# Optimization experiments

Measured on AMD Instinct MI355X. Metric: run time of the kernel, lower is better.

The kernel has to match this reference:

```python
import jax, jax.numpy as jnp
import numpy as np

N_NODES = 100000
N_EDGES = 1000000
N_FEAT = 136
HIDDEN = 64
N_CLASSES = 2
NUM_GRAPHS = 512


def setup_inputs() -> dict:
    key = jax.random.key(0)
    ks = jax.random.split(key, 8)
    x = jax.random.normal(ks[0], (N_NODES, N_FEAT), dtype=jnp.float32)
    edge_index = jax.random.randint(ks[1], (2, N_EDGES), 0, N_NODES, dtype=jnp.int64)
    batch = jnp.sort(jax.random.randint(ks[2], (N_NODES,), 0, NUM_GRAPHS, dtype=jnp.int64))
    W1 = jax.random.normal(ks[3], (N_FEAT, HIDDEN), dtype=jnp.float32) * (1.0 / np.sqrt(N_FEAT))
    b1 = jnp.zeros((HIDDEN,), dtype=jnp.float32)
    W2 = jax.random.normal(ks[4], (HIDDEN, HIDDEN), dtype=jnp.float32) * (1.0 / np.sqrt(HIDDEN))
    b2 = jnp.zeros((HIDDEN,), dtype=jnp.float32)
    Wout = jax.random.normal(ks[5], (HIDDEN, N_CLASSES), dtype=jnp.float32) * (1.0 / np.sqrt(HIDDEN))
    bout = jnp.zeros((N_CLASSES,), dtype=jnp.float32)
    return {"x": x, "edge_index": edge_index, "batch": batch,
            "W1": W1, "b1": b1, "W2": W2, "b2": b2, "Wout": Wout, "bout": bout}


def _gcn_conv(x, src, dst, W, b, n_nodes):
    # GCNConv: D^{-1/2} (A+I) D^{-1/2} X W + b (self-loops already appended in src/dst)
    h = x @ W                                           # [N, out]
    ones = jnp.ones(src.shape, dtype=h.dtype)
    deg = jax.ops.segment_sum(ones, dst, num_segments=n_nodes)  # in-degree incl. self-loop
    dinv = jnp.where(deg > 0, jax.lax.rsqrt(deg), 0.0)
    norm = dinv[src] * dinv[dst]                        # [E]
    msg = h[src] * norm[:, None]                        # gather + normalize
    out = jax.ops.segment_sum(msg, dst, num_segments=n_nodes)   # scatter-add
    return out + b


def reference(x, edge_index, batch, W1, b1, W2, b2, Wout, bout):
    n = x.shape[0]
    loops = jnp.arange(n, dtype=edge_index.dtype)
    src = jnp.concatenate([edge_index[0], loops])
    dst = jnp.concatenate([edge_index[1], loops])

    h = jax.nn.relu(_gcn_conv(x, src, dst, W1, b1, n))
    # dropout p=0.5 is identity in eval mode
    h = jax.nn.relu(_gcn_conv(h, src, dst, W2, b2, n))

    # global_mean_pool over batch segments
    sums = jax.ops.segment_sum(h, batch, num_segments=NUM_GRAPHS)       # [G, H]
    counts = jax.ops.segment_sum(jnp.ones((n,), h.dtype), batch, num_segments=NUM_GRAPHS)
    pooled = sums / jnp.maximum(counts, 1.0)[:, None]

    return pooled @ Wout + bout                                         # [G, C]
```

## Files before the change

### kernel.cpp

```cpp
#include <hip/hip_runtime.h>
#include <hip/hip_bf16.h>

#define N_NODES   100000
#define N_EDGES   1000000
#define N_FEAT    136
#define HIDDEN    64
#define N_CLASSES 2
#define NUM_GRAPHS 512

#define NP_PAD    100352
#define SCAN_BLKS 98

#define EPW       128
#define NWAVE     7813
#define E_PAD     (NWAVE * EPW)
#define SEG_BLOCKS ((NWAVE + 3) / 4)

#define K1_4 (N_FEAT / 4)
#define K2_4 (HIDDEN / 4)

#define K1PAD 160
#define K2PAD 72

#define NB_E    ((N_EDGES + 255) / 256)
#define NB_SC   ((N_EDGES / 4 + 255) / 256)
#define NB_HIST (NB_E + 3)
#define NB_MM   ((N_NODES + 63) / 64)
#define FUSED_GRID 5474

typedef unsigned short ushort_t;
typedef __attribute__((ext_vector_type(8))) short bf16x8;
typedef __attribute__((ext_vector_type(4))) float f32x4;
typedef __attribute__((ext_vector_type(4))) int i32x4;
typedef __attribute__((ext_vector_type(4))) unsigned short u16x4;

__device__ __forceinline__ ushort_t f2b(float v) {
    unsigned b = __float_as_uint(v);
    return (ushort_t)((b + 0x7FFF + ((b >> 16) & 1)) >> 16);
}
__device__ __forceinline__ float b2f(ushort_t u) {
    return __uint_as_float(((unsigned)u) << 16);
}
__device__ __forceinline__ unsigned pack2(float a, float b) {
    return (unsigned)f2b(a) | ((unsigned)f2b(b) << 16);
}

__global__ __launch_bounds__(256) void fused_hist_mm1_kernel(
        const int* __restrict__ dst, int* __restrict__ cnt,
        ushort_t* __restrict__ rank,
        const int* __restrict__ batch, int* __restrict__ gstart,
        const float* __restrict__ x, const float* __restrict__ W1,
        ushort_t* __restrict__ tpb) {
    __shared__ ushort_t wtb[64 * K1PAD];
    int t = threadIdx.x;
    int gq = blockIdx.x / 7, gr = blockIdx.x % 7;

    if (gr >= 2) {
        int hb = gq * 5 + (gr - 2);
        if (hb >= NB_HIST) return;
        if (hb >= NB_E) {
            int g = (hb - NB_E) * 256 + t;
            if (g <= NUM_GRAPHS) {
                int lo = 0, hi = N_NODES;
                while (lo < hi) {
                    int mid = (lo + hi) >> 1;
                    if (batch[mid] < g) lo = mid + 1; else hi = mid;
                }
                gstart[g] = lo;
            }
            return;
        }
        int e = hb * 256 + t;
        if (e < N_EDGES) {
            int d = __builtin_nontemporal_load(&dst[e]);
            int r = atomicAdd(&cnt[d], 1);
            __builtin_nontemporal_store((ushort_t)r, &rank[e]);
        }
        return;
    }

    int mb = gq * 2 + gr;
    if (mb >= NB_MM) return;
    int n0 = mb * 64;
    {
        for (int i = t; i < N_FEAT * HIDDEN; i += 256) {
            int n = i & 63, k = i >> 6;
            wtb[n * K1PAD + k] = f2b(W1[i]);
        }
        for (int i = t; i < 64 * 12; i += 256) {
            int n = i / 12, c = i % 12;
            *(unsigned*)&wtb[n * K1PAD + N_FEAT + 2 * c] = 0;
        }
    }
    __syncthreads();
    int w = t >> 6, lane = t & 63;
    int quad = lane >> 4, l16 = lane & 15;
    int an = n0 + w * 16 + l16; if (an >= N_NODES) an = N_NODES - 1;
    const f32x4* xr = (const f32x4*)(x + (long long)an * N_FEAT);
    f32x4 acc[4] = {{0,0,0,0},{0,0,0,0},{0,0,0,0},{0,0,0,0}};
#pragma unroll
    for (int kc = 0; kc < K1PAD / 32; ++kc) {
        int k0 = kc * 32 + quad * 8;
        bf16x8 a = {0, 0, 0, 0, 0, 0, 0, 0};
        if (k0 < N_FEAT) {
            f32x4 u0 = __builtin_nontemporal_load(&xr[kc * 8 + quad * 2]);
            f32x4 u1 = __builtin_nontemporal_load(&xr[kc * 8 + quad * 2 + 1]);
            union { bf16x8 v; unsigned u[4]; } cv;
            cv.u[0] = pack2(u0.x, u0.y);
            cv.u[1] = pack2(u0.z, u0.w);
            cv.u[2] = pack2(u1.x, u1.y);
            cv.u[3] = pack2(u1.z, u1.w);
            a = cv.v;
        }
#pragma unroll
        for (int nt = 0; nt < 4; ++nt) {
            bf16x8 b = *(const bf16x8*)&wtb[(nt * 16 + l16) * K1PAD + kc * 32 + quad * 8];
            acc[nt] = __builtin_amdgcn_mfma_f32_16x16x32_bf16(a, b, acc[nt], 0, 0, 0);
        }
    }
#pragma unroll
    for (int r = 0; r < 4; ++r) {
        int nl = w * 16 + quad * 4 + r;
        int node = n0 + nl;
        if (node < N_NODES) {
#pragma unroll
            for (int nt = 0; nt < 4; ++nt)
                tpb[node * 64 + nt * 16 + l16] = f2b(acc[nt][r]);
        }
    }
}

__global__ __launch_bounds__(256) void scan1_kernel(const int* __restrict__ cnt,
                                                    int* __restrict__ row_ptr,
                                                    int* __restrict__ partials) {
    __shared__ int sd[256];
    int b = blockIdx.x, t = threadIdx.x;
    int i0 = b * 1024 + t * 4;
    int c0 = (i0 + 0 < N_NODES) ? cnt[i0 + 0] : 0;
    int c1 = (i0 + 1 < N_NODES) ? cnt[i0 + 1] : 0;
    int c2 = (i0 + 2 < N_NODES) ? cnt[i0 + 2] : 0;
    int c3 = (i0 + 3 < N_NODES) ? cnt[i0 + 3] : 0;
    int tsum = c0 + c1 + c2 + c3;
    sd[t] = tsum;
    __syncthreads();
    for (int off = 1; off < 256; off <<= 1) {
        int v = (t >= off) ? sd[t - off] : 0;
        __syncthreads();
        sd[t] += v;
        __syncthreads();
    }
    int excl = sd[t] - tsum;
    row_ptr[i0 + 0] = excl;
    row_ptr[i0 + 1] = excl + c0;
    row_ptr[i0 + 2] = excl + c0 + c1;
    row_ptr[i0 + 3] = excl + c0 + c1 + c2;
    if (t == 255) partials[b] = sd[255];
}

__global__ __launch_bounds__(128) void scan2_kernel(int* __restrict__ partials) {
    __shared__ int sd[128];
    int t = threadIdx.x;
    int v = (t < SCAN_BLKS) ? partials[t] : 0;
    sd[t] = v;
    __syncthreads();
    for (int off = 1; off < 128; off <<= 1) {
        int u = (t >= off) ? sd[t - off] : 0;
        __syncthreads();
        sd[t] += u;
        __syncthreads();
    }
    partials[t] = sd[t] - v;
}

__global__ __launch_bounds__(256) void scan3_kernel(int* __restrict__ row_ptr,
                                                    const int* __restrict__ cnt,
                                                    const int* __restrict__ partials,
                                                    int* __restrict__ dst_sorted,
                                                    int* __restrict__ csr_src,
                                                    float* __restrict__ dinv) {
    int i = blockIdx.x * 256 + threadIdx.x;
    if (i < N_NODES) {
        int v = row_ptr[i] + partials[i >> 10];
        int deg = cnt[i];
        row_ptr[i] = v;
        dinv[i] = rsqrtf((float)(deg + 1));
        for (int j = v; j < v + deg; ++j) dst_sorted[j] = i;
    }
    if (i == N_NODES) {
        row_ptr[N_NODES] = N_EDGES;
        for (int j = N_EDGES; j < E_PAD; ++j) {
            dst_sorted[j] = N_NODES;
            csr_src[j] = 0;
        }
    }
}

__global__ __launch_bounds__(256) void scatter_kernel(const int* __restrict__ src,
                                                      const int* __restrict__ dst,
                                                      const ushort_t* __restrict__ rank,
                                                      const int* __restrict__ row_ptr,
                                                      int* __restrict__ csr_src) {
    int e0 = (blockIdx.x * 256 + threadIdx.x) * 4;
    if (e0 >= N_EDGES) return;
    i32x4 s4 = __builtin_nontemporal_load((const i32x4*)&src[e0]);
    i32x4 d4 = __builtin_nontemporal_load((const i32x4*)&dst[e0]);
    u16x4 r4 = *(const u16x4*)&rank[e0];
    int p0 = row_ptr[d4.x] + (int)r4.x;
    int p1 = row_ptr[d4.y] + (int)r4.y;
    int p2 = row_ptr[d4.z] + (int)r4.z;
    int p3 = row_ptr[d4.w] + (int)r4.w;
    csr_src[p0] = s4.x;
    csr_src[p1] = s4.y;
    csr_src[p2] = s4.z;
    csr_src[p3] = s4.w;
}

__global__ __launch_bounds__(256) void mm2_kernel(float* __restrict__ agg,
                                                  ushort_t* __restrict__ tpb,
                                                  const float* __restrict__ W2,
                                                  const float* __restrict__ dinv,
                                                  const float* __restrict__ bias) {
    __shared__ ushort_t hsb[64 * K2PAD];
    __shared__ ushort_t wtb[64 * K2PAD];
    __shared__ float    dsv[64];
    __shared__ float    bsv[64];
    int t = threadIdx.x;
    int n0 = blockIdx.x * 64;
    if (t < 64) {
        int n = n0 + t; if (n >= N_NODES) n = N_NODES - 1;
        dsv[t] = dinv[n];
        bsv[t] = bias[t];
    }
    __syncthreads();
    {
        for (int i = t; i < HIDDEN * HIDDEN; i += 256) {
            int n = i & 63, k = i >> 6;
            wtb[n * K2PAD + k] = f2b(W2[i]);
        }
        for (int i = t; i < 64 * 4; i += 256) {
            int n = i / 4, c = i % 4;
            *(unsigned*)&wtb[n * K2PAD + HIDDEN + 2 * c] = 0;
        }
        for (int i = t; i < 64 * 16; i += 256) {
            int r = i >> 4, c = i & 15;
            int n_raw = n0 + r;
            int n = (n_raw < N_NODES) ? n_raw : N_NODES - 1;
            float4 va = ((const float4*)agg)[n * 16 + c];
            uint2 ut = *(const uint2*)&tpb[n * 64 + c * 4];
            float di = dsv[r];
            float s0 = b2f((ushort_t)(ut.x & 0xffff)) * di;
            float s1 = b2f((ushort_t)(ut.x >> 16)) * di;
            float s2 = b2f((ushort_t)(ut.y & 0xffff)) * di;
            float s3 = b2f((ushort_t)(ut.y >> 16)) * di;
            float h0 = fmaxf(fmaf(va.x + s0, di, bsv[c * 4 + 0]), 0.f);
            float h1 = fmaxf(fmaf(va.y + s1, di, bsv[c * 4 + 1]), 0.f);
            float h2 = fmaxf(fmaf(va.z + s2, di, bsv[c * 4 + 2]), 0.f);
            float h3 = fmaxf(fmaf(va.w + s3, di, bsv[c * 4 + 3]), 0.f);
            *(uint2*)&hsb[r * K2PAD + 4 * c] = make_uint2(pack2(h0, h1), pack2(h2, h3));
            if (n_raw < N_NODES)
                ((float4*)agg)[n * 16 + c] = make_float4(0.f, 0.f, 0.f, 0.f);
        }
        for (int i = t; i < 64 * 4; i += 256) {
            int r = i / 4, c = i % 4;
            *(unsigned*)&hsb[r * K2PAD + HIDDEN + 2 * c] = 0;
        }
    }
    __syncthreads();
    int w = t >> 6, lane = t & 63;
    int quad = lane >> 4, l16 = lane & 15;
    f32x4 acc[4] = {{0,0,0,0},{0,0,0,0},{0,0,0,0},{0,0,0,0}};
#pragma unroll
    for (int kc = 0; kc < 2; ++kc) {
        bf16x8 a = *(const bf16x8*)&hsb[(w * 16 + l16) * K2PAD + kc * 32 + quad * 8];
#pragma unroll
        for (int nt = 0; nt < 4; ++nt) {
            bf16x8 b = *(const bf16x8*)&wtb[(nt * 16 + l16) * K2PAD + kc * 32 + quad * 8];
            acc[nt] = __builtin_amdgcn_mfma_f32_16x16x32_bf16(a, b, acc[nt], 0, 0, 0);
        }
    }
#pragma unroll
    for (int r = 0; r < 4; ++r) {
        int nl = w * 16 + quad * 4 + r;
        int node = n0 + nl;
        if (node < N_NODES) {
            float di = dsv[nl];
#pragma unroll
            for (int nt = 0; nt < 4; ++nt)
                tpb[node * 64 + nt * 16 + l16] = f2b(acc[nt][r] * di);
        }
    }
}

template<bool SCALE_SRC>
__global__ __launch_bounds__(256, 4) void edge_seg_kernel(const int* __restrict__ csr_src,
                                                          const int* __restrict__ dst_sorted,
                                                          const ushort_t* __restrict__ tpb,
                                                          const float* __restrict__ dinv,
                                                          float* __restrict__ agg) {
    int lane = threadIdx.x & 63;
    int wid  = (blockIdx.x * 256 + threadIdx.x) >> 6;
    if (wid >= NWAVE) return;
    int e0 = wid * EPW;

    int sv0 = csr_src[e0 + lane],      sv1 = csr_src[e0 + 64 + lane];
    int dv0 = dst_sorted[e0 + lane],   dv1 = dst_sorted[e0 + 64 + lane];

    float acc = 0.0f;
    int dprev = __builtin_amdgcn_readlane(dv0, 0);
    int nflush = 0;
#pragma unroll
    for (int j = 0; j < 8; ++j) {
        int svj = (j < 4) ? sv0 : sv1;
        int dvj = (j < 4) ? dv0 : dv1;
        int base = (j * 16) & 63;
        int ss[16], dd[16];
#pragma unroll
        for (int k = 0; k < 16; ++k) {
            ss[k] = __builtin_amdgcn_readlane(svj, base + k);
            dd[k] = __builtin_amdgcn_readlane(dvj, base + k);
        }
        float vv[16];
#pragma unroll
        for (int k = 0; k < 16; ++k) {
            float v = b2f(tpb[ss[k] * 64 + lane]);
            if (SCALE_SRC) v *= dinv[ss[k]];
            vv[k] = v;
        }
#pragma unroll
        for (int k = 0; k < 16; ++k) {
            if (dd[k] != dprev) {
                if (nflush == 0) atomicAdd(&agg[dprev * 64 + lane], acc);
                else             agg[dprev * 64 + lane] = acc;
                ++nflush;
                acc = 0.0f;
                dprev = dd[k];
            }
            acc += vv[k];
        }
    }
    atomicAdd(&agg[dprev * 64 + lane], acc);
}

__global__ __launch_bounds__(256) void gpool_kernel(const float* __restrict__ agg,
                                                    const ushort_t* __restrict__ tpb,
                                                    const float* __restrict__ dinv,
                                                    const float* __restrict__ bias,
                                                    const int* __restrict__ gstart,
                                                    const float* __restrict__ Wout,
                                                    const float* __restrict__ bout,
                                                    float* __restrict__ out) {
    __shared__ float red[4][64];
    int lane = threadIdx.x & 63;
    int w = threadIdx.x >> 6;
    int g = blockIdx.x;
    int s = gstart[g], e = gstart[g + 1];
    float b = bias[lane];
    float acc = 0.0f;
    for (int n = s + w; n < e; n += 4) {
        int idx = n * 64 + lane;
        acc += fmaxf(fmaf(agg[idx] + b2f(tpb[idx]), dinv[n], b), 0.0f);
    }
    red[w][lane] = acc;
    __syncthreads();
    if (threadIdx.x < 64) {
        float tot = red[0][lane] + red[1][lane] + red[2][lane] + red[3][lane];
        float p = tot / fmaxf((float)(e - s), 1.0f);
        float c0 = p * Wout[lane * N_CLASSES + 0];
        float c1 = p * Wout[lane * N_CLASSES + 1];
#pragma unroll
        for (int off = 32; off > 0; off >>= 1) {
            c0 += __shfl_down(c0, off);
            c1 += __shfl_down(c1, off);
        }
        if (lane == 0) {
            out[g * N_CLASSES + 0] = c0 + bout[0];
            out[g * N_CLASSES + 1] = c1 + bout[1];
        }
    }
}

extern "C" void kernel_launch(void* const* d_in, const int* in_sizes, int n_in,
                              void* d_out, int out_size, void* d_ws, size_t ws_size,
                              hipStream_t stream) {
    const float* x     = (const float*)d_in[0];
    const int*   ei    = (const int*)d_in[1];
    const int*   batch = (const int*)d_in[2];
    const float* W1    = (const float*)d_in[3];
    const float* b1    = (const float*)d_in[4];
    const float* W2    = (const float*)d_in[5];
    const float* b2    = (const float*)d_in[6];
    const float* Wout  = (const float*)d_in[7];
    const float* bout  = (const float*)d_in[8];
    float* out = (float*)d_out;

    const int* src = ei;
    const int* dst = ei + N_EDGES;

    char* p = (char*)d_ws;
    int*      row_ptr   = (int*)p;      p += (NP_PAD + 256) * sizeof(int);
    int*      cnt       = (int*)p;      p += NP_PAD * sizeof(int);
    int*      partials  = (int*)p;      p += 256 * sizeof(int);
    int*      gstart    = (int*)p;      p += (NUM_GRAPHS + 64) * sizeof(int);
    int*      csr_src   = (int*)p;      p += (size_t)E_PAD * sizeof(int);
    int*      dst_sorted= (int*)p;      p += (size_t)E_PAD * sizeof(int);
    float*    dinv      = (float*)p;    p += NP_PAD * sizeof(float);
    ushort_t* tpb       = (ushort_t*)p; p += (size_t)N_NODES * HIDDEN * sizeof(ushort_t);
    float*    agg       = (float*)p;    p += (size_t)(N_NODES + 1) * HIDDEN * sizeof(float);
    ushort_t* rank16    = (ushort_t*)agg;

    hipMemsetAsync(cnt, 0, NP_PAD * sizeof(int), stream);
    fused_hist_mm1_kernel<<<FUSED_GRID, 256, 0, stream>>>(dst, cnt, rank16,
                                                          batch, gstart,
                                                          x, W1, tpb);
    scan1_kernel<<<SCAN_BLKS, 256, 0, stream>>>(cnt, row_ptr, partials);
    scan2_kernel<<<1, 128, 0, stream>>>(partials);
    scan3_kernel<<<NP_PAD / 256 + 1, 256, 0, stream>>>(row_ptr, cnt, partials,
                                                       dst_sorted, csr_src, dinv);
    scatter_kernel<<<NB_SC, 256, 0, stream>>>(src, dst, rank16, row_ptr, csr_src);

    hipMemsetAsync(agg, 0, (size_t)(N_NODES + 1) * HIDDEN * sizeof(float), stream);

    edge_seg_kernel<true><<<SEG_BLOCKS, 256, 0, stream>>>(csr_src, dst_sorted,
                                                          tpb, dinv, agg);

    mm2_kernel<<<NB_MM, 256, 0, stream>>>(agg, tpb, W2, dinv, b1);
    edge_seg_kernel<false><<<SEG_BLOCKS, 256, 0, stream>>>(csr_src, dst_sorted,
                                                           tpb, dinv, agg);

    gpool_kernel<<<NUM_GRAPHS, 256, 0, stream>>>(agg, tpb, dinv, b2, gstart,
                                                 Wout, bout, out);
}
```

Measured before the change: 269.0 us.

## Replace edge-segment atomic aggregation with per-node CSR pull gathers fused into mm2

The edge-balanced segmented reduction with atomics and the dst_sorted array go away. Each wave now pulls a destination node's neighbours through row_ptr/csr_src and accumulates in registers. Layer-1 aggregation is fused into the mm2 kernel, and layer-2 aggregation writes finished bf16 activations that pooling reads directly. This removes the float agg buffer, its memset, the atomics and the dst_sorted fill loop. The cost is that work is now split per node rather than per edge, so uneven degrees can load-balance poorly, and each mm2 block runs 16 serial gathers per wave before its MFMA stage.

```diff
diff --git a/kernel.cpp b/kernel.cpp
--- a/kernel.cpp
+++ b/kernel.cpp
@@ -11,10 +11,7 @@
 #define NP_PAD    100352
 #define SCAN_BLKS 98
 
-#define EPW       128
-#define NWAVE     7813
-#define E_PAD     (NWAVE * EPW)
-#define SEG_BLOCKS ((NWAVE + 3) / 4)
+#define E_PAD     1000064
 
 #define K1_4 (N_FEAT / 4)
 #define K2_4 (HIDDEN / 4)
@@ -175,24 +172,14 @@
 __global__ __launch_bounds__(256) void scan3_kernel(int* __restrict__ row_ptr,
                                                     const int* __restrict__ cnt,
                                                     const int* __restrict__ partials,
-                                                    int* __restrict__ dst_sorted,
-                                                    int* __restrict__ csr_src,
                                                     float* __restrict__ dinv) {
     int i = blockIdx.x * 256 + threadIdx.x;
     if (i < N_NODES) {
         int v = row_ptr[i] + partials[i >> 10];
-        int deg = cnt[i];
         row_ptr[i] = v;
-        dinv[i] = rsqrtf((float)(deg + 1));
-        for (int j = v; j < v + deg; ++j) dst_sorted[j] = i;
-    }
-    if (i == N_NODES) {
-        row_ptr[N_NODES] = N_EDGES;
-        for (int j = N_EDGES; j < E_PAD; ++j) {
-            dst_sorted[j] = N_NODES;
-            csr_src[j] = 0;
-        }
-    }
+        dinv[i] = rsqrtf((float)(cnt[i] + 1));
+    }
+    if (i == N_NODES) row_ptr[N_NODES] = N_EDGES;
 }
 
 __global__ __launch_bounds__(256) void scatter_kernel(const int* __restrict__ src,
@@ -215,58 +202,53 @@
     csr_src[p3] = s4.w;
 }
 
-__global__ __launch_bounds__(256) void mm2_kernel(float* __restrict__ agg,
-                                                  ushort_t* __restrict__ tpb,
-                                                  const float* __restrict__ W2,
-                                                  const float* __restrict__ dinv,
-                                                  const float* __restrict__ bias) {
+__global__ __launch_bounds__(256) void mm2agg_kernel(
+        const int* __restrict__ row_ptr, const int* __restrict__ csr_src,
+        const ushort_t* __restrict__ tpb,
+        const float* __restrict__ dinv,
+        const float* __restrict__ W2, const float* __restrict__ bias,
+        ushort_t* __restrict__ tpb2) {
     __shared__ ushort_t hsb[64 * K2PAD];
     __shared__ ushort_t wtb[64 * K2PAD];
-    __shared__ float    dsv[64];
-    __shared__ float    bsv[64];
     int t = threadIdx.x;
     int n0 = blockIdx.x * 64;
-    if (t < 64) {
-        int n = n0 + t; if (n >= N_NODES) n = N_NODES - 1;
-        dsv[t] = dinv[n];
-        bsv[t] = bias[t];
-    }
-    __syncthreads();
-    {
-        for (int i = t; i < HIDDEN * HIDDEN; i += 256) {
-            int n = i & 63, k = i >> 6;
-            wtb[n * K2PAD + k] = f2b(W2[i]);
-        }
-        for (int i = t; i < 64 * 4; i += 256) {
-            int n = i / 4, c = i % 4;
-            *(unsigned*)&wtb[n * K2PAD + HIDDEN + 2 * c] = 0;
-        }
-        for (int i = t; i < 64 * 16; i += 256) {
-            int r = i >> 4, c = i & 15;
-            int n_raw = n0 + r;
-            int n = (n_raw < N_NODES) ? n_raw : N_NODES - 1;
-            float4 va = ((const float4*)agg)[n * 16 + c];
-            uint2 ut = *(const uint2*)&tpb[n * 64 + c * 4];
-            float di = dsv[r];
-            float s0 = b2f((ushort_t)(ut.x & 0xffff)) * di;
-            float s1 = b2f((ushort_t)(ut.x >> 16)) * di;
-            float s2 = b2f((ushort_t)(ut.y & 0xffff)) * di;
-            float s3 = b2f((ushort_t)(ut.y >> 16)) * di;
-            float h0 = fmaxf(fmaf(va.x + s0, di, bsv[c * 4 + 0]), 0.f);
-            float h1 = fmaxf(fmaf(va.y + s1, di, bsv[c * 4 + 1]), 0.f);
-            float h2 = fmaxf(fmaf(va.z + s2, di, bsv[c * 4 + 2]), 0.f);
-            float h3 = fmaxf(fmaf(va.w + s3, di, bsv[c * 4 + 3]), 0.f);
-            *(uint2*)&hsb[r * K2PAD + 4 * c] = make_uint2(pack2(h0, h1), pack2(h2, h3));
-            if (n_raw < N_NODES)
-                ((float4*)agg)[n * 16 + c] = make_float4(0.f, 0.f, 0.f, 0.f);
-        }
-        for (int i = t; i < 64 * 4; i += 256) {
-            int r = i / 4, c = i % 4;
-            *(unsigned*)&hsb[r * K2PAD + HIDDEN + 2 * c] = 0;
-        }
-    }
-    __syncthreads();
+    for (int i = t; i < HIDDEN * HIDDEN; i += 256) {
+        int n = i & 63, k = i >> 6;
+        wtb[n * K2PAD + k] = f2b(W2[i]);
+    }
+    for (int i = t; i < 64 * 4; i += 256) {
+        int n = i / 4, c = i % 4;
+        *(unsigned*)&wtb[n * K2PAD + HIDDEN + 2 * c] = 0;
+        *(unsigned*)&hsb[n * K2PAD + HIDDEN + 2 * c] = 0;
+    }
     int w = t >> 6, lane = t & 63;
+    float bl = bias[lane];
+    for (int nl = 0; nl < 16; ++nl) {
+        int n_raw = n0 + w * 16 + nl;
+        int n = (n_raw < N_NODES) ? n_raw : N_NODES - 1;
+        int r0 = row_ptr[n], r1 = row_ptr[n + 1];
+        float a = 0.0f;
+        for (int base = r0; base < r1; base += 64) {
+            int cnt = r1 - base; if (cnt > 64) cnt = 64;
+            int sv = csr_src[base + (lane < cnt ? lane : cnt - 1)];
+            int j = 0;
+            for (; j + 1 < cnt; j += 2) {
+                int s0 = __builtin_amdgcn_readlane(sv, j);
+                int s1 = __builtin_amdgcn_readlane(sv, j + 1);
+                float v0 = dinv[s0] * b2f(tpb[(size_t)s0 * 64 + lane]);
+                float v1 = dinv[s1] * b2f(tpb[(size_t)s1 * 64 + lane]);
+                a += v0 + v1;
+            }
+            if (j < cnt) {
+                int s0 = __builtin_amdgcn_readlane(sv, j);
+                a += dinv[s0] * b2f(tpb[(size_t)s0 * 64 + lane]);
+            }
+        }
+        float dn = dinv[n];
+        float h = fmaxf(fmaf(fmaf(dn, b2f(tpb[(size_t)n * 64 + lane]), a), dn, bl), 0.f);
+        hsb[(w * 16 + nl) * K2PAD + lane] = f2b(h);
+    }
+    __syncthreads();
     int quad = lane >> 4, l16 = lane & 15;
     f32x4 acc[4] = {{0,0,0,0},{0,0,0,0},{0,0,0,0},{0,0,0,0}};
 #pragma unroll
@@ -283,68 +265,50 @@
         int nl = w * 16 + quad * 4 + r;
         int node = n0 + nl;
         if (node < N_NODES) {
-            float di = dsv[nl];
+            float di = dinv[node];
 #pragma unroll
             for (int nt = 0; nt < 4; ++nt)
-                tpb[node * 64 + nt * 16 + l16] = f2b(acc[nt][r] * di);
-        }
-    }
-}
-
-template<bool SCALE_SRC>
-__global__ __launch_bounds__(256, 4) void edge_seg_kernel(const int* __restrict__ csr_src,
-                                                          const int* __restrict__ dst_sorted,
-                                                          const ushort_t* __restrict__ tpb,
-                                                          const float* __restrict__ dinv,
-                                                          float* __restrict__ agg) {
-    int lane = threadIdx.x & 63;
-    int wid  = (blockIdx.x * 256 + threadIdx.x) >> 6;
-    if (wid >= NWAVE) return;
-    int e0 = wid * EPW;
-
-    int sv0 = csr_src[e0 + lane],      sv1 = csr_src[e0 + 64 + lane];
-    int dv0 = dst_sorted[e0 + lane],   dv1 = dst_sorted[e0 + 64 + lane];
-
-    float acc = 0.0f;
-    int dprev = __builtin_amdgcn_readlane(dv0, 0);
-    int nflush = 0;
-#pragma unroll
-    for (int j = 0; j < 8; ++j) {
-        int svj = (j < 4) ? sv0 : sv1;
-        int dvj = (j < 4) ? dv0 : dv1;
-        int base = (j * 16) & 63;
-        int ss[16], dd[16];
-#pragma unroll
-        for (int k = 0; k < 16; ++k) {
-            ss[k] = __builtin_amdgcn_readlane(svj, base + k);
-            dd[k] = __builtin_amdgcn_readlane(dvj, base + k);
-        }
-        float vv[16];
-#pragma unroll
-        for (int k = 0; k < 16; ++k) {
-            float v = b2f(tpb[ss[k] * 64 + lane]);
-            if (SCALE_SRC) v *= dinv[ss[k]];
-            vv[k] = v;
-        }
-#pragma unroll
-        for (int k = 0; k < 16; ++k) {
-            if (dd[k] != dprev) {
-                if (nflush == 0) atomicAdd(&agg[dprev * 64 + lane], acc);
-                else             agg[dprev * 64 + lane] = acc;
-                ++nflush;
-                acc = 0.0f;
-                dprev = dd[k];
-            }
-            acc += vv[k];
-        }
-    }
-    atomicAdd(&agg[dprev * 64 + lane], acc);
-}
-
-__global__ __launch_bounds__(256) void gpool_kernel(const float* __restrict__ agg,
-                                                    const ushort_t* __restrict__ tpb,
-                                                    const float* __restrict__ dinv,
-                                                    const float* __restrict__ bias,
+                tpb2[node * 64 + nt * 16 + l16] = f2b(acc[nt][r] * di);
+        }
+    }
+}
+
+__global__ __launch_bounds__(256) void agg2_kernel(
+        const int* __restrict__ row_ptr, const int* __restrict__ csr_src,
+        const ushort_t* __restrict__ tpb2, const float* __restrict__ dinv,
+        const float* __restrict__ bias, ushort_t* __restrict__ h2) {
+    int t = threadIdx.x;
+    int n0 = blockIdx.x * 64;
+    int w = t >> 6, lane = t & 63;
+    float bl = bias[lane];
+    for (int nl = 0; nl < 16; ++nl) {
+        int n = n0 + w * 16 + nl;
+        if (n >= N_NODES) break;
+        int r0 = row_ptr[n], r1 = row_ptr[n + 1];
+        float a = 0.0f;
+        for (int base = r0; base < r1; base += 64) {
+            int cnt = r1 - base; if (cnt > 64) cnt = 64;
+            int sv = csr_src[base + (lane < cnt ? lane : cnt - 1)];
+            int j = 0;
+            for (; j + 1 < cnt; j += 2) {
+                int s0 = __builtin_amdgcn_readlane(sv, j);
+                int s1 = __builtin_amdgcn_readlane(sv, j + 1);
+                float v0 = b2f(tpb2[(size_t)s0 * 64 + lane]);
+                float v1 = b2f(tpb2[(size_t)s1 * 64 + lane]);
+                a += v0 + v1;
+            }
+            if (j < cnt) {
+                int s0 = __builtin_amdgcn_readlane(sv, j);
+                a += b2f(tpb2[(size_t)s0 * 64 + lane]);
+            }
+        }
+        float dn = dinv[n];
+        float h = fmaxf(fmaf(a + b2f(tpb2[(size_t)n * 64 + lane]), dn, bl), 0.f);
+        h2[(size_t)n * 64 + lane] = f2b(h);
+    }
+}
+
+__global__ __launch_bounds__(256) void gpool_kernel(const ushort_t* __restrict__ h2,
                                                     const int* __restrict__ gstart,
                                                     const float* __restrict__ Wout,
                                                     const float* __restrict__ bout,
@@ -354,12 +318,9 @@
     int w = threadIdx.x >> 6;
     int g = blockIdx.x;
     int s = gstart[g], e = gstart[g + 1];
-    float b = bias[lane];
     float acc = 0.0f;
-    for (int n = s + w; n < e; n += 4) {
-        int idx = n * 64 + lane;
-        acc += fmaxf(fmaf(agg[idx] + b2f(tpb[idx]), dinv[n], b), 0.0f);
-    }
+    for (int n = s + w; n < e; n += 4)
+        acc += b2f(h2[(size_t)n * 64 + lane]);
     red[w][lane] = acc;
     __syncthreads();
     if (threadIdx.x < 64) {
@@ -402,11 +363,11 @@
     int*      partials  = (int*)p;      p += 256 * sizeof(int);
     int*      gstart    = (int*)p;      p += (NUM_GRAPHS + 64) * sizeof(int);
     int*      csr_src   = (int*)p;      p += (size_t)E_PAD * sizeof(int);
-    int*      dst_sorted= (int*)p;      p += (size_t)E_PAD * sizeof(int);
     float*    dinv      = (float*)p;    p += NP_PAD * sizeof(float);
     ushort_t* tpb       = (ushort_t*)p; p += (size_t)N_NODES * HIDDEN * sizeof(ushort_t);
-    float*    agg       = (float*)p;    p += (size_t)(N_NODES + 1) * HIDDEN * sizeof(float);
-    ushort_t* rank16    = (ushort_t*)agg;
+    ushort_t* tpb2      = (ushort_t*)p; p += (size_t)N_NODES * HIDDEN * sizeof(ushort_t);
+    ushort_t* rank16    = (ushort_t*)tpb2;
+    ushort_t* h2        = tpb;
 
     hipMemsetAsync(cnt, 0, NP_PAD * sizeof(int), stream);
     fused_hist_mm1_kernel<<<FUSED_GRID, 256, 0, stream>>>(dst, cnt, rank16,
@@ -414,19 +375,12 @@
                                                           x, W1, tpb);
     scan1_kernel<<<SCAN_BLKS, 256, 0, stream>>>(cnt, row_ptr, partials);
     scan2_kernel<<<1, 128, 0, stream>>>(partials);
-    scan3_kernel<<<NP_PAD / 256 + 1, 256, 0, stream>>>(row_ptr, cnt, partials,
-                                                       dst_sorted, csr_src, dinv);
+    scan3_kernel<<<NP_PAD / 256 + 1, 256, 0, stream>>>(row_ptr, cnt, partials, dinv);
     scatter_kernel<<<NB_SC, 256, 0, stream>>>(src, dst, rank16, row_ptr, csr_src);
 
-    hipMemsetAsync(agg, 0, (size_t)(N_NODES + 1) * HIDDEN * sizeof(float), stream);
-
-    edge_seg_kernel<true><<<SEG_BLOCKS, 256, 0, stream>>>(csr_src, dst_sorted,
-                                                          tpb, dinv, agg);
-
-    mm2_kernel<<<NB_MM, 256, 0, stream>>>(agg, tpb, W2, dinv, b1);
-    edge_seg_kernel<false><<<SEG_BLOCKS, 256, 0, stream>>>(csr_src, dst_sorted,
-                                                           tpb, dinv, agg);
-
-    gpool_kernel<<<NUM_GRAPHS, 256, 0, stream>>>(agg, tpb, dinv, b2, gstart,
-                                                 Wout, bout, out);
-}
+    mm2agg_kernel<<<NB_MM, 256, 0, stream>>>(row_ptr, csr_src, tpb, dinv,
+                                             W2, b1, tpb2);
+    agg2_kernel<<<NB_MM, 256, 0, stream>>>(row_ptr, csr_src, tpb2, dinv, b2, h2);
+
+    gpool_kernel<<<NUM_GRAPHS, 256, 0, stream>>>(h2, gstart, Wout, bout, out);
+}
```

Measured after the change: 312.7 us. +16.3%, slower.

## Replace global-atomic degree histogram with chunked shared-memory counts and column scan

Applied to the files above, without the earlier changes.

The edge in-degree histogram moves from global atomics into LDS atomics. Edges are split into 32 chunks and nodes into 8 ranges, and each block histograms one chunk/range pair and writes per-chunk 8-bit counts. A new column-scan kernel turns these into per-chunk prefixes and total degrees, and scatter adds the chunk prefix to the rank. This removes the cnt memset and global atomic contention, at the cost of every partition block rereading its dst chunk 8 times, an extra kernel launch, a 3.2MB byte array, and 8-bit counts that overflow if a node gets more than 255 edges in one chunk.

```diff
diff --git a/kernel.cpp b/kernel.cpp
--- a/kernel.cpp
+++ b/kernel.cpp
@@ -17,18 +17,22 @@
 #define SEG_BLOCKS ((NWAVE + 3) / 4)
 
 #define K1_4 (N_FEAT / 4)
-#define K2_4 (HIDDEN / 4)
-
 #define K1PAD 160
 #define K2PAD 72
 
-#define NB_E    ((N_EDGES + 255) / 256)
 #define NB_SC   ((N_EDGES / 4 + 255) / 256)
-#define NB_HIST (NB_E + 3)
 #define NB_MM   ((N_NODES + 63) / 64)
-#define FUSED_GRID 5474
+
+#define NCH   32
+#define CHK   (N_EDGES / NCH)
+#define NRG   8
+#define RNG   (N_NODES / NRG)
+#define NP1   (NCH * NRG)
+#define NGB   3
+#define FUSED_GRID (NP1 + NGB + NB_MM)
 
 typedef unsigned short ushort_t;
+typedef unsigned char u8_t;
 typedef __attribute__((ext_vector_type(8))) short bf16x8;
 typedef __attribute__((ext_vector_type(4))) float f32x4;
 typedef __attribute__((ext_vector_type(4))) int i32x4;
@@ -45,42 +49,52 @@
     return (unsigned)f2b(a) | ((unsigned)f2b(b) << 16);
 }
 
-__global__ __launch_bounds__(256) void fused_hist_mm1_kernel(
-        const int* __restrict__ dst, int* __restrict__ cnt,
-        ushort_t* __restrict__ rank,
+__global__ __launch_bounds__(256) void fused_csr_mm1_kernel(
+        const int* __restrict__ dst,
+        ushort_t* __restrict__ rank, u8_t* __restrict__ chunkcnt,
         const int* __restrict__ batch, int* __restrict__ gstart,
         const float* __restrict__ x, const float* __restrict__ W1,
         ushort_t* __restrict__ tpb) {
-    __shared__ ushort_t wtb[64 * K1PAD];
+    __shared__ __align__(16) char smem_u[RNG * 4];
     int t = threadIdx.x;
-    int gq = blockIdx.x / 7, gr = blockIdx.x % 7;
-
-    if (gr >= 2) {
-        int hb = gq * 5 + (gr - 2);
-        if (hb >= NB_HIST) return;
-        if (hb >= NB_E) {
-            int g = (hb - NB_E) * 256 + t;
-            if (g <= NUM_GRAPHS) {
-                int lo = 0, hi = N_NODES;
-                while (lo < hi) {
-                    int mid = (lo + hi) >> 1;
-                    if (batch[mid] < g) lo = mid + 1; else hi = mid;
-                }
-                gstart[g] = lo;
+    int bid = blockIdx.x;
+
+    if (bid < NP1) {
+        int* lh = (int*)smem_u;
+        int c = bid >> 3, r = bid & 7;
+        for (int i = t; i < RNG; i += 256) lh[i] = 0;
+        __syncthreads();
+        int e0 = c * CHK;
+        int lo = r * RNG;
+        for (int i = t; i < CHK; i += 256) {
+            int e = e0 + i;
+            int d = __builtin_nontemporal_load(&dst[e]) - lo;
+            if ((unsigned)d < (unsigned)RNG) {
+                int rk = atomicAdd(&lh[d], 1);
+                rank[e] = (ushort_t)rk;
             }
-            return;
-        }
-        int e = hb * 256 + t;
-        if (e < N_EDGES) {
-            int d = __builtin_nontemporal_load(&dst[e]);
-            int r = atomicAdd(&cnt[d], 1);
-            __builtin_nontemporal_store((ushort_t)r, &rank[e]);
-        }
+        }
+        __syncthreads();
+        u8_t* cc = &chunkcnt[(size_t)c * N_NODES + lo];
+        for (int i = t; i < RNG; i += 256) cc[i] = (u8_t)lh[i];
         return;
     }
 
-    int mb = gq * 2 + gr;
-    if (mb >= NB_MM) return;
+    if (bid < NP1 + NGB) {
+        int g = (bid - NP1) * 256 + t;
+        if (g <= NUM_GRAPHS) {
+            int lo = 0, hi = N_NODES;
+            while (lo < hi) {
+                int mid = (lo + hi) >> 1;
+                if (batch[mid] < g) lo = mid + 1; else hi = mid;
+            }
+            gstart[g] = lo;
+        }
+        return;
+    }
+
+    ushort_t* wtb = (ushort_t*)smem_u;
+    int mb = bid - NP1 - NGB;
     int n0 = mb * 64;
     {
         for (int i = t; i < N_FEAT * HIDDEN; i += 256) {
@@ -128,6 +142,21 @@
                 tpb[node * 64 + nt * 16 + l16] = f2b(acc[nt][r]);
         }
     }
+}
+
+__global__ __launch_bounds__(256) void colscan_kernel(u8_t* __restrict__ chunkcnt,
+                                                      int* __restrict__ cnt) {
+    int d = blockIdx.x * 256 + threadIdx.x;
+    if (d >= N_NODES) return;
+    int s = 0;
+#pragma unroll
+    for (int c = 0; c < NCH; ++c) {
+        size_t idx = (size_t)c * N_NODES + d;
+        int v = chunkcnt[idx];
+        chunkcnt[idx] = (u8_t)s;
+        s += v;
+    }
+    cnt[d] = s;
 }
 
 __global__ __launch_bounds__(256) void scan1_kernel(const int* __restrict__ cnt,
@@ -198,6 +227,7 @@
 __global__ __launch_bounds__(256) void scatter_kernel(const int* __restrict__ src,
                                                       const int* __restrict__ dst,
                                                       const ushort_t* __restrict__ rank,
+                                                      const u8_t* __restrict__ chunkpre,
                                                       const int* __restrict__ row_ptr,
                                                       int* __restrict__ csr_src) {
     int e0 = (blockIdx.x * 256 + threadIdx.x) * 4;
@@ -205,10 +235,12 @@
     i32x4 s4 = __builtin_nontemporal_load((const i32x4*)&src[e0]);
     i32x4 d4 = __builtin_nontemporal_load((const i32x4*)&dst[e0]);
     u16x4 r4 = *(const u16x4*)&rank[e0];
-    int p0 = row_ptr[d4.x] + (int)r4.x;
-    int p1 = row_ptr[d4.y] + (int)r4.y;
-    int p2 = row_ptr[d4.z] + (int)r4.z;
-    int p3 = row_ptr[d4.w] + (int)r4.w;
+    int c0 = (e0 + 0) / CHK, c1 = (e0 + 1) / CHK;
+    int c2 = (e0 + 2) / CHK, c3 = (e0 + 3) / CHK;
+    int p0 = row_ptr[d4.x] + (int)chunkpre[(size_t)c0 * N_NODES + d4.x] + (int)r4.x;
+    int p1 = row_ptr[d4.y] + (int)chunkpre[(size_t)c1 * N_NODES + d4.y] + (int)r4.y;
+    int p2 = row_ptr[d4.z] + (int)chunkpre[(size_t)c2 * N_NODES + d4.z] + (int)r4.z;
+    int p3 = row_ptr[d4.w] + (int)chunkpre[(size_t)c3 * N_NODES + d4.w] + (int)r4.w;
     csr_src[p0] = s4.x;
     csr_src[p1] = s4.y;
     csr_src[p2] = s4.z;
@@ -407,16 +439,18 @@
     ushort_t* tpb       = (ushort_t*)p; p += (size_t)N_NODES * HIDDEN * sizeof(ushort_t);
     float*    agg       = (float*)p;    p += (size_t)(N_NODES + 1) * HIDDEN * sizeof(float);
     ushort_t* rank16    = (ushort_t*)agg;
-
-    hipMemsetAsync(cnt, 0, NP_PAD * sizeof(int), stream);
-    fused_hist_mm1_kernel<<<FUSED_GRID, 256, 0, stream>>>(dst, cnt, rank16,
-                                                          batch, gstart,
-                                                          x, W1, tpb);
+    u8_t*     chunkcnt  = (u8_t*)agg + (size_t)E_PAD * sizeof(ushort_t);
+
+    fused_csr_mm1_kernel<<<FUSED_GRID, 256, 0, stream>>>(dst, rank16, chunkcnt,
+                                                         batch, gstart,
+                                                         x, W1, tpb);
+    colscan_kernel<<<(N_NODES + 255) / 256, 256, 0, stream>>>(chunkcnt, cnt);
     scan1_kernel<<<SCAN_BLKS, 256, 0, stream>>>(cnt, row_ptr, partials);
     scan2_kernel<<<1, 128, 0, stream>>>(partials);
     scan3_kernel<<<NP_PAD / 256 + 1, 256, 0, stream>>>(row_ptr, cnt, partials,
                                                        dst_sorted, csr_src, dinv);
-    scatter_kernel<<<NB_SC, 256, 0, stream>>>(src, dst, rank16, row_ptr, csr_src);
+    scatter_kernel<<<NB_SC, 256, 0, stream>>>(src, dst, rank16, chunkcnt,
+                                              row_ptr, csr_src);
 
     hipMemsetAsync(agg, 0, (size_t)(N_NODES + 1) * HIDDEN * sizeof(float), stream);
 
```

Result: slower. 306.6 us (+14.0%).

## Fuse CSR aggregation into node-tile kernels with LDS accumulation, drop atomics

Applied to the files above, without the earlier changes.

Replaces the edge-balanced segmented-reduction kernels, which flushed into a global fp32 accumulator with atomics, with node-tile kernels. Each wave gathers the CSR range of its 16 destination nodes into a shared-memory tile. Layer-1 aggregation is fused with the W2 MFMA matmul, layer-2 aggregation is fused with bias and ReLU into a bf16 h2 buffer, and pooling then just reads h2. This removes the large agg memset, the global atomics and the fp32 agg traffic. In exchange, work per wave now follows the per-node degree distribution, so load balance can be worse than fixed 128-edge chunks.

```diff
diff --git a/kernel.cpp b/kernel.cpp
--- a/kernel.cpp
+++ b/kernel.cpp
@@ -11,14 +11,9 @@
 #define NP_PAD    100352
 #define SCAN_BLKS 98
 
-#define EPW       128
-#define NWAVE     7813
-#define E_PAD     (NWAVE * EPW)
-#define SEG_BLOCKS ((NWAVE + 3) / 4)
+#define E_PAD     1000064
 
 #define K1_4 (N_FEAT / 4)
-#define K2_4 (HIDDEN / 4)
-
 #define K1PAD 160
 #define K2PAD 72
 
@@ -215,58 +210,112 @@
     csr_src[p3] = s4.w;
 }
 
-__global__ __launch_bounds__(256) void mm2_kernel(float* __restrict__ agg,
-                                                  ushort_t* __restrict__ tpb,
-                                                  const float* __restrict__ W2,
-                                                  const float* __restrict__ dinv,
-                                                  const float* __restrict__ bias) {
+template<bool SCALE_SRC>
+__device__ __forceinline__ void tile_gather(const int* __restrict__ csr_src,
+                                            const int* __restrict__ dst_sorted,
+                                            const ushort_t* __restrict__ table,
+                                            const float* __restrict__ dinv,
+                                            float* __restrict__ hagg, int n0,
+                                            int a, int b, int lane) {
+    if (a >= b) return;
+    float acc = 0.0f;
+    int dprev = 0;
+    for (int base = a; base < b; base += 64) {
+        int cnt = b - base; if (cnt > 64) cnt = 64;
+        int sv = csr_src[base + lane];
+        int dv = dst_sorted[base + lane];
+        if (base == a) dprev = __builtin_amdgcn_readlane(dv, 0);
+#pragma unroll
+        for (int j = 0; j < 4; ++j) {
+            int kbase = j * 16;
+            if (kbase >= cnt) break;
+            int kmax = cnt - kbase; if (kmax > 16) kmax = 16;
+            int ss[16], dd[16];
+#pragma unroll
+            for (int k = 0; k < 16; ++k) {
+                ss[k] = __builtin_amdgcn_readlane(sv, kbase + k);
+                dd[k] = __builtin_amdgcn_readlane(dv, kbase + k);
+            }
+            float vv[16];
+#pragma unroll
+            for (int k = 0; k < 16; ++k) {
+                if (k < kmax) {
+                    float v = b2f(table[(size_t)ss[k] * 64 + lane]);
+                    if (SCALE_SRC) v *= dinv[ss[k]];
+                    vv[k] = v;
+                }
+            }
+#pragma unroll
+            for (int k = 0; k < 16; ++k) {
+                if (k < kmax) {
+                    if (dd[k] != dprev) {
+                        hagg[(dprev - n0) * 64 + lane] = acc;
+                        acc = 0.0f;
+                        dprev = dd[k];
+                    }
+                    acc += vv[k];
+                }
+            }
+        }
+    }
+    hagg[(dprev - n0) * 64 + lane] = acc;
+}
+
+__global__ __launch_bounds__(256) void aggmm2_kernel(
+        const int* __restrict__ row_ptr, const int* __restrict__ csr_src,
+        const int* __restrict__ dst_sorted,
+        const ushort_t* __restrict__ tpb, const float* __restrict__ dinv,
+        const float* __restrict__ W2, const float* __restrict__ bias,
+        ushort_t* __restrict__ tpb2) {
+    __shared__ __align__(16) float hagg[64 * 64];
     __shared__ ushort_t hsb[64 * K2PAD];
     __shared__ ushort_t wtb[64 * K2PAD];
     __shared__ float    dsv[64];
     __shared__ float    bsv[64];
     int t = threadIdx.x;
     int n0 = blockIdx.x * 64;
+    int w = t >> 6, lane = t & 63;
+#pragma unroll
+    for (int r = 0; r < 16; ++r) hagg[(w * 16 + r) * 64 + lane] = 0.f;
     if (t < 64) {
         int n = n0 + t; if (n >= N_NODES) n = N_NODES - 1;
         dsv[t] = dinv[n];
         bsv[t] = bias[t];
     }
-    __syncthreads();
-    {
-        for (int i = t; i < HIDDEN * HIDDEN; i += 256) {
-            int n = i & 63, k = i >> 6;
-            wtb[n * K2PAD + k] = f2b(W2[i]);
-        }
-        for (int i = t; i < 64 * 4; i += 256) {
-            int n = i / 4, c = i % 4;
-            *(unsigned*)&wtb[n * K2PAD + HIDDEN + 2 * c] = 0;
-        }
-        for (int i = t; i < 64 * 16; i += 256) {
-            int r = i >> 4, c = i & 15;
-            int n_raw = n0 + r;
-            int n = (n_raw < N_NODES) ? n_raw : N_NODES - 1;
-            float4 va = ((const float4*)agg)[n * 16 + c];
-            uint2 ut = *(const uint2*)&tpb[n * 64 + c * 4];
-            float di = dsv[r];
-            float s0 = b2f((ushort_t)(ut.x & 0xffff)) * di;
-            float s1 = b2f((ushort_t)(ut.x >> 16)) * di;
-            float s2 = b2f((ushort_t)(ut.y & 0xffff)) * di;
-            float s3 = b2f((ushort_t)(ut.y >> 16)) * di;
-            float h0 = fmaxf(fmaf(va.x + s0, di, bsv[c * 4 + 0]), 0.f);
-            float h1 = fmaxf(fmaf(va.y + s1, di, bsv[c * 4 + 1]), 0.f);
-            float h2 = fmaxf(fmaf(va.z + s2, di, bsv[c * 4 + 2]), 0.f);
-            float h3 = fmaxf(fmaf(va.w + s3, di, bsv[c * 4 + 3]), 0.f);
-            *(uint2*)&hsb[r * K2PAD + 4 * c] = make_uint2(pack2(h0, h1), pack2(h2, h3));
-            if (n_raw < N_NODES)
-                ((float4*)agg)[n * 16 + c] = make_float4(0.f, 0.f, 0.f, 0.f);
-        }
-        for (int i = t; i < 64 * 4; i += 256) {
-            int r = i / 4, c = i % 4;
-            *(unsigned*)&hsb[r * K2PAD + HIDDEN + 2 * c] = 0;
-        }
-    }
-    __syncthreads();
-    int w = t >> 6, lane = t & 63;
+    for (int i = t; i < HIDDEN * HIDDEN; i += 256) {
+        int n = i & 63, k = i >> 6;
+        wtb[n * K2PAD + k] = f2b(W2[i]);
+    }
+    for (int i = t; i < 64 * 4; i += 256) {
+        int n = i / 4, c = i % 4;
+        *(unsigned*)&wtb[n * K2PAD + HIDDEN + 2 * c] = 0;
+        *(unsigned*)&hsb[n * K2PAD + HIDDEN + 2 * c] = 0;
+    }
+    int m0 = n0 + w * 16;
+    if (m0 < N_NODES) {
+        int m1 = m0 + 16; if (m1 > N_NODES) m1 = N_NODES;
+        int a = row_ptr[m0], b = row_ptr[m1];
+        tile_gather<true>(csr_src, dst_sorted, tpb, dinv, hagg, n0, a, b, lane);
+    }
+    __syncthreads();
+    for (int i = t; i < 64 * 16; i += 256) {
+        int r = i >> 4, c = i & 15;
+        int n_raw = n0 + r;
+        int n = (n_raw < N_NODES) ? n_raw : N_NODES - 1;
+        float4 va = *(const float4*)&hagg[r * 64 + c * 4];
+        uint2 ut = *(const uint2*)&tpb[(size_t)n * 64 + c * 4];
+        float di = dsv[r];
+        float s0 = b2f((ushort_t)(ut.x & 0xffff)) * di;
+        float s1 = b2f((ushort_t)(ut.x >> 16)) * di;
+        float s2 = b2f((ushort_t)(ut.y & 0xffff)) * di;
+        float s3 = b2f((ushort_t)(ut.y >> 16)) * di;
+        float h0 = fmaxf(fmaf(va.x + s0, di, bsv[c * 4 + 0]), 0.f);
+        float h1 = fmaxf(fmaf(va.y + s1, di, bsv[c * 4 + 1]), 0.f);
+        float h2 = fmaxf(fmaf(va.z + s2, di, bsv[c * 4 + 2]), 0.f);
+        float h3 = fmaxf(fmaf(va.w + s3, di, bsv[c * 4 + 3]), 0.f);
+        *(uint2*)&hsb[r * K2PAD + 4 * c] = make_uint2(pack2(h0, h1), pack2(h2, h3));
+    }
+    __syncthreads();
     int quad = lane >> 4, l16 = lane & 15;
     f32x4 acc[4] = {{0,0,0,0},{0,0,0,0},{0,0,0,0},{0,0,0,0}};
 #pragma unroll
@@ -286,65 +335,41 @@
             float di = dsv[nl];
 #pragma unroll
             for (int nt = 0; nt < 4; ++nt)
-                tpb[node * 64 + nt * 16 + l16] = f2b(acc[nt][r] * di);
-        }
-    }
-}
-
-template<bool SCALE_SRC>
-__global__ __launch_bounds__(256, 4) void edge_seg_kernel(const int* __restrict__ csr_src,
-                                                          const int* __restrict__ dst_sorted,
-                                                          const ushort_t* __restrict__ tpb,
-                                                          const float* __restrict__ dinv,
-                                                          float* __restrict__ agg) {
-    int lane = threadIdx.x & 63;
-    int wid  = (blockIdx.x * 256 + threadIdx.x) >> 6;
-    if (wid >= NWAVE) return;
-    int e0 = wid * EPW;
-
-    int sv0 = csr_src[e0 + lane],      sv1 = csr_src[e0 + 64 + lane];
-    int dv0 = dst_sorted[e0 + lane],   dv1 = dst_sorted[e0 + 64 + lane];
-
-    float acc = 0.0f;
-    int dprev = __builtin_amdgcn_readlane(dv0, 0);
-    int nflush = 0;
-#pragma unroll
-    for (int j = 0; j < 8; ++j) {
-        int svj = (j < 4) ? sv0 : sv1;
-        int dvj = (j < 4) ? dv0 : dv1;
-        int base = (j * 16) & 63;
-        int ss[16], dd[16];
-#pragma unroll
-        for (int k = 0; k < 16; ++k) {
-            ss[k] = __builtin_amdgcn_readlane(svj, base + k);
-            dd[k] = __builtin_amdgcn_readlane(dvj, base + k);
-        }
-        float vv[16];
-#pragma unroll
-        for (int k = 0; k < 16; ++k) {
-            float v = b2f(tpb[ss[k] * 64 + lane]);
-            if (SCALE_SRC) v *= dinv[ss[k]];
-            vv[k] = v;
-        }
-#pragma unroll
-        for (int k = 0; k < 16; ++k) {
-            if (dd[k] != dprev) {
-                if (nflush == 0) atomicAdd(&agg[dprev * 64 + lane], acc);
-                else             agg[dprev * 64 + lane] = acc;
-                ++nflush;
-                acc = 0.0f;
-                dprev = dd[k];
-            }
-            acc += vv[k];
-        }
-    }
-    atomicAdd(&agg[dprev * 64 + lane], acc);
-}
-
-__global__ __launch_bounds__(256) void gpool_kernel(const float* __restrict__ agg,
-                                                    const ushort_t* __restrict__ tpb,
-                                                    const float* __restrict__ dinv,
-                                                    const float* __restrict__ bias,
+                tpb2[(size_t)node * 64 + nt * 16 + l16] = f2b(acc[nt][r] * di);
+        }
+    }
+}
+
+__global__ __launch_bounds__(256) void agg2_kernel(
+        const int* __restrict__ row_ptr, const int* __restrict__ csr_src,
+        const int* __restrict__ dst_sorted,
+        const ushort_t* __restrict__ tpb2, const float* __restrict__ dinv,
+        const float* __restrict__ bias, ushort_t* __restrict__ h2) {
+    __shared__ __align__(16) float hagg[64 * 64];
+    int t = threadIdx.x;
+    int n0 = blockIdx.x * 64;
+    int w = t >> 6, lane = t & 63;
+#pragma unroll
+    for (int r = 0; r < 16; ++r) hagg[(w * 16 + r) * 64 + lane] = 0.f;
+    int m0 = n0 + w * 16;
+    if (m0 < N_NODES) {
+        int m1 = m0 + 16; if (m1 > N_NODES) m1 = N_NODES;
+        int a = row_ptr[m0], b = row_ptr[m1];
+        tile_gather<false>(csr_src, dst_sorted, tpb2, dinv, hagg, n0, a, b, lane);
+    }
+    __syncthreads();
+    float bl = bias[lane];
+    for (int r = w; r < 64; r += 4) {
+        int n = n0 + r;
+        if (n >= N_NODES) break;
+        float dn = dinv[n];
+        float va = hagg[r * 64 + lane];
+        float h = fmaxf(fmaf(va + b2f(tpb2[(size_t)n * 64 + lane]), dn, bl), 0.f);
+        h2[(size_t)n * 64 + lane] = f2b(h);
+    }
+}
+
+__global__ __launch_bounds__(256) void gpool_kernel(const ushort_t* __restrict__ h2,
                                                     const int* __restrict__ gstart,
                                                     const float* __restrict__ Wout,
                                                     const float* __restrict__ bout,
@@ -354,12 +379,9 @@
     int w = threadIdx.x >> 6;
     int g = blockIdx.x;
     int s = gstart[g], e = gstart[g + 1];
-    float b = bias[lane];
     float acc = 0.0f;
-    for (int n = s + w; n < e; n += 4) {
-        int idx = n * 64 + lane;
-        acc += fmaxf(fmaf(agg[idx] + b2f(tpb[idx]), dinv[n], b), 0.0f);
-    }
+    for (int n = s + w; n < e; n += 4)
+        acc += b2f(h2[(size_t)n * 64 + lane]);
     red[w][lane] = acc;
     __syncthreads();
     if (threadIdx.x < 64) {
@@ -405,8 +427,9 @@
     int*      dst_sorted= (int*)p;      p += (size_t)E_PAD * sizeof(int);
     float*    dinv      = (float*)p;    p += NP_PAD * sizeof(float);
     ushort_t* tpb       = (ushort_t*)p; p += (size_t)N_NODES * HIDDEN * sizeof(ushort_t);
-    float*    agg       = (float*)p;    p += (size_t)(N_NODES + 1) * HIDDEN * sizeof(float);
-    ushort_t* rank16    = (ushort_t*)agg;
+    ushort_t* tpb2      = (ushort_t*)p; p += (size_t)N_NODES * HIDDEN * sizeof(ushort_t);
+    ushort_t* rank16    = (ushort_t*)tpb2;
+    ushort_t* h2        = tpb;
 
     hipMemsetAsync(cnt, 0, NP_PAD * sizeof(int), stream);
     fused_hist_mm1_kernel<<<FUSED_GRID, 256, 0, stream>>>(dst, cnt, rank16,
@@ -418,15 +441,10 @@
                                                        dst_sorted, csr_src, dinv);
     scatter_kernel<<<NB_SC, 256, 0, stream>>>(src, dst, rank16, row_ptr, csr_src);
 
-    hipMemsetAsync(agg, 0, (size_t)(N_NODES + 1) * HIDDEN * sizeof(float), stream);
-
-    edge_seg_kernel<true><<<SEG_BLOCKS, 256, 0, stream>>>(csr_src, dst_sorted,
-                                                          tpb, dinv, agg);
-
-    mm2_kernel<<<NB_MM, 256, 0, stream>>>(agg, tpb, W2, dinv, b1);
-    edge_seg_kernel<false><<<SEG_BLOCKS, 256, 0, stream>>>(csr_src, dst_sorted,
-                                                           tpb, dinv, agg);
-
-    gpool_kernel<<<NUM_GRAPHS, 256, 0, stream>>>(agg, tpb, dinv, b2, gstart,
-                                                 Wout, bout, out);
-}
+    aggmm2_kernel<<<NB_MM, 256, 0, stream>>>(row_ptr, csr_src, dst_sorted,
+                                             tpb, dinv, W2, b1, tpb2);
+    agg2_kernel<<<NB_MM, 256, 0, stream>>>(row_ptr, csr_src, dst_sorted,
+                                           tpb2, dinv, b2, h2);
+
+    gpool_kernel<<<NUM_GRAPHS, 256, 0, stream>>>(h2, gstart, Wout, bout, out);
+}
```

New measurement: 401.3 us. 1.49x slower.
